# Kernel optimization log

Hardware: AMD Instinct MI355X
Metric: run time of the kernel (lower is better)

Reference implementation:

```python
import jax, jax.numpy as jnp
import numpy as np

SEQ_LEN, N_FEAT, EMB = 512, 8, 64
HID = 2 * EMB  # 128
BATCH = 512


def _lstm_layer(x, Wih, Whh, bih, bhh):
    """Single-layer LSTM, batch_first x: [B,T,F]. PyTorch gate order i,f,g,o.
    Returns (outputs [B,T,H], final hidden [B,H])."""
    B = x.shape[0]
    H = Whh.shape[1]
    # precompute input projections for all timesteps: [B,T,4H]
    xp = jnp.einsum('btf,gf->btg', x, Wih) + bih + bhh

    def step(carry, xt):
        h, c = carry
        gates = xt + h @ Whh.T  # [B,4H]
        i, f, g, o = jnp.split(gates, 4, axis=-1)
        i = jax.nn.sigmoid(i)
        f = jax.nn.sigmoid(f)
        g = jnp.tanh(g)
        o = jax.nn.sigmoid(o)
        c = f * c + i * g
        h = o * jnp.tanh(c)
        return (h, c), h

    h0 = jnp.zeros((B, H), dtype=x.dtype)
    c0 = jnp.zeros((B, H), dtype=x.dtype)
    (hT, _), hs = jax.lax.scan(step, (h0, c0), xp.transpose(1, 0, 2))
    return hs.transpose(1, 0, 2), hT


def setup_inputs() -> dict:
    key = jax.random.key(0)
    ks = jax.random.split(key, 13)
    inp = {"x": jax.random.normal(ks[0], (BATCH, SEQ_LEN, N_FEAT), dtype=jnp.float32)}

    def mk(k, shape, fan):
        s = 1.0 / np.sqrt(fan)
        return jax.random.uniform(k, shape, dtype=jnp.float32, minval=-s, maxval=s)

    # layer 1: in=N_FEAT, hid=HID
    inp["Wih1"] = mk(ks[1], (4 * HID, N_FEAT), HID)
    inp["Whh1"] = mk(ks[2], (4 * HID, HID), HID)
    inp["bih1"] = mk(ks[3], (4 * HID,), HID)
    inp["bhh1"] = mk(ks[4], (4 * HID,), HID)
    # layer 2: in=HID, hid=HID
    inp["Wih2"] = mk(ks[5], (4 * HID, HID), HID)
    inp["Whh2"] = mk(ks[6], (4 * HID, HID), HID)
    inp["bih2"] = mk(ks[7], (4 * HID,), HID)
    inp["bhh2"] = mk(ks[8], (4 * HID,), HID)
    # layer 3: in=HID, hid=EMB
    inp["Wih3"] = mk(ks[9], (4 * EMB, HID), EMB)
    inp["Whh3"] = mk(ks[10], (4 * EMB, EMB), EMB)
    inp["bih3"] = mk(ks[11], (4 * EMB,), EMB)
    inp["bhh3"] = mk(ks[12], (4 * EMB,), EMB)
    return inp


def reference(x, Wih1, Whh1, bih1, bhh1, Wih2, Whh2, bih2, bhh2, Wih3, Whh3, bih3, bhh3):
    B = x.shape[0]
    x = x.reshape(B, SEQ_LEN, N_FEAT)
    x, _ = _lstm_layer(x, Wih1, Whh1, bih1, bhh1)
    x, _ = _lstm_layer(x, Wih2, Whh2, bih2, bhh2)
    _, hT = _lstm_layer(x, Wih3, Whh3, bih3, bhh3)
    return hT  # [B, EMB]
```

## Files before the change

kernel.cpp:

```cpp
#include <hip/hip_runtime.h>


#define DEVI __device__ __forceinline__

typedef _Float16 h8 __attribute__((ext_vector_type(8)));
typedef float f4 __attribute__((ext_vector_type(4)));

static constexpr int T_ = 512, TC_ = 16, NC_ = T_ / TC_;

DEVI float sigmoidf_(float x) {
    return __builtin_amdgcn_rcpf(1.f + __builtin_amdgcn_exp2f(x * -1.44269504f));
}
DEVI float tanhf_(float x) {
    return 2.f * __builtin_amdgcn_rcpf(1.f + __builtin_amdgcn_exp2f(x * -2.88539008f)) - 1.f;
}

DEVI h8 cvt8(const float* p) {
    const float4 a = *reinterpret_cast<const float4*>(p);
    const float4 b = *reinterpret_cast<const float4*>(p + 4);
    return h8{(_Float16)a.x, (_Float16)a.y, (_Float16)a.z, (_Float16)a.w,
              (_Float16)b.x, (_Float16)b.y, (_Float16)b.z, (_Float16)b.w};
}

DEVI void lds_barrier() {
    asm volatile("s_waitcnt lgkmcnt(0)\n\ts_barrier" ::: "memory");
}

template <int LAYER>
DEVI void stage(int tile, char* smem, const float* x, const _Float16* Oin,
                _Float16* Oout, const float* Wih, const float* Whh,
                const float* bih, const float* bhh, float* out,
                int* flag_in, int* flag_out) {
    constexpr int H = (LAYER == 3) ? 64 : 128;
    constexpr int KT_H = H / 32;
    constexpr int KT_X = (LAYER == 1) ? 1 : 4;
    constexpr int HP = H + 8;
    constexpr int NWAVE = (LAYER == 3) ? 4 : 8;

    const int tid  = threadIdx.x;
    const int lane = tid & 63;
    const int wv   = tid >> 6;
    const int lr   = lane & 15;
    const int lk   = lane >> 4;
    const int b0   = tile * 16;
    const bool active = (wv < NWAVE);
    const int jcol = (wv & (NWAVE - 1)) * 16 + lr;

    _Float16 (*h_lds)[16][HP] = (_Float16 (*)[16][HP])smem;

    h8 wbh[4][KT_H], wbx[4][KT_X];
    float bias[4];
    if (active) {
#pragma unroll
        for (int q = 0; q < 4; q++) {
#pragma unroll
            for (int kt = 0; kt < KT_H; kt++)
                wbh[q][kt] = cvt8(Whh + (size_t)(q * H + jcol) * H + kt * 32 + lk * 8);
            if constexpr (LAYER == 1) {
                wbx[q][0] = (lk == 0) ? cvt8(Wih + (size_t)(q * H + jcol) * 8) : h8{};
            } else {
#pragma unroll
                for (int kt = 0; kt < KT_X; kt++)
                    wbx[q][kt] = cvt8(Wih + (size_t)(q * H + jcol) * 128 + kt * 32 + lk * 8);
            }
            bias[q] = bih[q * H + jcol] + bhh[q * H + jcol];
        }
    }

    float c[4] = {0.f, 0.f, 0.f, 0.f};

    for (int i = tid; i < 2 * 16 * HP; i += 512) ((_Float16*)smem)[i] = (_Float16)0;
    __syncthreads();

    auto load_x = [&](int t, h8* xa) {
        if constexpr (LAYER == 1) {
            xa[0] = (lk == 0) ? cvt8(x + ((size_t)(b0 + lr) * T_ + t) * 8) : h8{};
        } else {
#pragma unroll
            for (int kt = 0; kt < KT_X; kt++)
                xa[kt] = *reinterpret_cast<const h8*>(
                    Oin + ((size_t)(b0 + lr) * T_ + t) * 128 + kt * 32 + lk * 8);
        }
    };

    auto xmfma = [&](const h8* xv, f4* ax) {
#pragma unroll
        for (int q = 0; q < 4; q++) ax[q] = f4{bias[q], bias[q], bias[q], bias[q]};
#pragma unroll
        for (int kt = 0; kt < KT_X; kt++)
#pragma unroll
            for (int q = 0; q < 4; q++)
                ax[q] = __builtin_amdgcn_mfma_f32_16x16x32_f16(xv[kt], wbx[q][kt], ax[q], 0, 0, 0);
    };

    h8 xa[KT_X], xb[KT_X];
    f4 accA[4], accB[4];

#define STEP_BODY(T_EXPR, TT, CUR, ACCU, ACCN, XLOAD, XPROJ)                              \
    {                                                                                     \
        const int t = (T_EXPR);                                                           \
        h8 ha[KT_H];                                                                      \
        _Pragma("unroll")                                                                 \
        for (int kt = 0; kt < KT_H; kt++)                                                 \
            ha[kt] = *reinterpret_cast<const h8*>(&h_lds[CUR][lr][kt * 32 + lk * 8]);     \
        _Pragma("unroll")                                                                 \
        for (int kt = 0; kt < KT_H; kt++)                                                 \
            _Pragma("unroll")                                                             \
            for (int q = 0; q < 4; q++)                                                   \
                ACCU[q] = __builtin_amdgcn_mfma_f32_16x16x32_f16(ha[kt], wbh[q][kt],      \
                                                                 ACCU[q], 0, 0, 0);       \
        if ((TT) + 2 < TC_) load_x(t + 2, XLOAD);          \
        _Pragma("unroll")                                                                 \
        for (int i = 0; i < 4; i++) {                                                     \
            const float gi = sigmoidf_(ACCU[0][i]);                                       \
            const float gf = sigmoidf_(ACCU[1][i]);                                       \
            const float gg = tanhf_(ACCU[2][i]);                                          \
            const float go = sigmoidf_(ACCU[3][i]);                                       \
            c[i] = gf * c[i] + gi * gg;                                                   \
            const float h = go * tanhf_(c[i]);                                            \
            const int row = lk * 4 + i;                                                   \
            h_lds[(CUR) ^ 1][row][jcol] = (_Float16)h;                                    \
            if constexpr (LAYER < 3) {                                                    \
                Oout[((size_t)(b0 + row) * T_ + t) * 128 + jcol] = (_Float16)h;           \
            } else {                                                                      \
                if (t == T_ - 1) out[(size_t)(b0 + row) * 64 + jcol] = h;                 \
            }                                                                             \
        }                                                                                 \
        if ((TT) + 1 < TC_) xmfma(XPROJ, ACCN);   \
    }

    for (int ch = 0; ch < NC_; ch++) {
        if constexpr (LAYER > 1) {
            if (tid == 0) {
                while (__hip_atomic_load(flag_in, __ATOMIC_RELAXED,
                                         __HIP_MEMORY_SCOPE_AGENT) < ch + 1)
                    __builtin_amdgcn_s_sleep(2);
                __threadfence();
            }
            __syncthreads();
        }
        const int t0 = ch * TC_;
        if (active) {
            load_x(t0, xa);
            load_x(t0 + 1, xb);
            xmfma(xa, accA);
        }

        for (int tb = 0; tb < TC_ / 2; tb++) {
            if (active) STEP_BODY(t0 + 2 * tb, 2 * tb, 0, accA, accB, xa, xb);
            lds_barrier();
            if (active) STEP_BODY(t0 + 2 * tb + 1, 2 * tb + 1, 1, accB, accA, xb, xa);
            lds_barrier();
        }

        if constexpr (LAYER < 3) {
            asm volatile("s_waitcnt vmcnt(0)" ::: "memory");
            __syncthreads();
            if (tid == 0) {
                __threadfence();
                __hip_atomic_store(flag_out, ch + 1, __ATOMIC_RELAXED,
                                   __HIP_MEMORY_SCOPE_AGENT);
            }
        }
    }
#undef STEP_BODY
}

__global__ __launch_bounds__(512, 1)
void mega_k(const float* __restrict__ x,
            const float* __restrict__ Wih1, const float* __restrict__ Whh1,
            const float* __restrict__ bih1, const float* __restrict__ bhh1,
            const float* __restrict__ Wih2, const float* __restrict__ Whh2,
            const float* __restrict__ bih2, const float* __restrict__ bhh2,
            const float* __restrict__ Wih3, const float* __restrict__ Whh3,
            const float* __restrict__ bih3, const float* __restrict__ bhh3,
            _Float16* __restrict__ O1, _Float16* __restrict__ O2,
            float* __restrict__ out, int* __restrict__ flags) {
    extern __shared__ char smem[];
    const int bid = blockIdx.x;
    if (bid < 32) {
        stage<1>(bid, smem, x, nullptr, O1, Wih1, Whh1, bih1, bhh1, nullptr,
                 nullptr, flags + bid);
    } else if (bid < 64) {
        stage<2>(bid - 32, smem, nullptr, O1, O2, Wih2, Whh2, bih2, bhh2, nullptr,
                 flags + (bid - 32), flags + 32 + (bid - 32));
    } else {
        stage<3>(bid - 64, smem, nullptr, O2, nullptr, Wih3, Whh3, bih3, bhh3, out,
                 flags + 32 + (bid - 64), nullptr);
    }
}

__global__ void zero_flags_k(int* flags) {
    if (threadIdx.x < 64)
        __hip_atomic_store(flags + threadIdx.x, 0, __ATOMIC_RELAXED,
                           __HIP_MEMORY_SCOPE_AGENT);
}

extern "C" void kernel_launch(void* const* d_in, const int* in_sizes, int n_in,
                              void* d_out, int out_size, void* d_ws, size_t ws_size,
                              hipStream_t stream) {
    const float* x = (const float*)d_in[0];
    float* out = (float*)d_out;

    char* ws = (char*)d_ws;
    _Float16* O1 = (_Float16*)ws;
    _Float16* O2 = (_Float16*)(ws + (size_t)67108864);
    int* flags   = (int*)(ws + (size_t)134217728);
    (void)ws_size; (void)in_sizes; (void)n_in; (void)out_size;

    zero_flags_k<<<1, 64, 0, stream>>>(flags);
    mega_k<<<96, 512, 8704, stream>>>(
        x,
        (const float*)d_in[1], (const float*)d_in[2], (const float*)d_in[3], (const float*)d_in[4],
        (const float*)d_in[5], (const float*)d_in[6], (const float*)d_in[7], (const float*)d_in[8],
        (const float*)d_in[9], (const float*)d_in[10], (const float*)d_in[11], (const float*)d_in[12],
        O1, O2, out, flags);
}
```

Before: 723.4 us.

## Process two batch tiles per block to interleave independent LSTM recurrences

```diff
diff --git a/kernel.cpp b/kernel.cpp
--- a/kernel.cpp
+++ b/kernel.cpp
@@ -27,26 +27,28 @@
 }
 
 template <int LAYER>
-DEVI void stage(int tile, char* smem, const float* x, const _Float16* Oin,
-                _Float16* Oout, const float* Wih, const float* Whh,
-                const float* bih, const float* bhh, float* out,
-                int* flag_in, int* flag_out) {
+DEVI void stage2(int tA, int tB, char* smem, const float* x, const _Float16* Oin,
+                 _Float16* Oout, const float* Wih, const float* Whh,
+                 const float* bih, const float* bhh, float* out,
+                 int* flin_base, int* flout_base) {
     constexpr int H = (LAYER == 3) ? 64 : 128;
     constexpr int KT_H = H / 32;
     constexpr int KT_X = (LAYER == 1) ? 1 : 4;
     constexpr int HP = H + 8;
     constexpr int NWAVE = (LAYER == 3) ? 4 : 8;
+    constexpr int LBUF = 2 * 16 * HP;
 
     const int tid  = threadIdx.x;
     const int lane = tid & 63;
     const int wv   = tid >> 6;
     const int lr   = lane & 15;
     const int lk   = lane >> 4;
-    const int b0   = tile * 16;
     const bool active = (wv < NWAVE);
     const int jcol = (wv & (NWAVE - 1)) * 16 + lr;
-
-    _Float16 (*h_lds)[16][HP] = (_Float16 (*)[16][HP])smem;
+    const int bA = tA * 16, bB = tB * 16;
+
+    _Float16 (*hldsA)[16][HP] = (_Float16 (*)[16][HP])smem;
+    _Float16 (*hldsB)[16][HP] = (_Float16 (*)[16][HP])(smem + LBUF * 2);
 
     h8 wbh[4][KT_H], wbx[4][KT_X];
     float bias[4];
@@ -67,12 +69,12 @@
         }
     }
 
-    float c[4] = {0.f, 0.f, 0.f, 0.f};
-
-    for (int i = tid; i < 2 * 16 * HP; i += 512) ((_Float16*)smem)[i] = (_Float16)0;
+    float cA[4] = {0.f, 0.f, 0.f, 0.f}, cB[4] = {0.f, 0.f, 0.f, 0.f};
+
+    for (int i = tid; i < 2 * LBUF; i += 512) ((_Float16*)smem)[i] = (_Float16)0;
     __syncthreads();
 
-    auto load_x = [&](int t, h8* xa) {
+    auto load_x = [&](int b0, int t, h8* xa) {
         if constexpr (LAYER == 1) {
             xa[0] = (lk == 0) ? cvt8(x + ((size_t)(b0 + lr) * T_ + t) * 8) : h8{};
         } else {
@@ -93,46 +95,71 @@
                 ax[q] = __builtin_amdgcn_mfma_f32_16x16x32_f16(xv[kt], wbx[q][kt], ax[q], 0, 0, 0);
     };
 
-    h8 xa[KT_X], xb[KT_X];
+    h8 xsA[KT_X], xsB[KT_X];
     f4 accA[4], accB[4];
 
-#define STEP_BODY(T_EXPR, TT, CUR, ACCU, ACCN, XLOAD, XPROJ)                              \
+#define STEP2(T_EXPR, TT, CUR)                                                            \
     {                                                                                     \
         const int t = (T_EXPR);                                                           \
-        h8 ha[KT_H];                                                                      \
+                   \
+        if ((TT) + 1 < TC_) { load_x(bA, t + 1, xsA); load_x(bB, t + 1, xsB); }           \
+        h8 haA[KT_H], haB[KT_H];                                                          \
         _Pragma("unroll")                                                                 \
-        for (int kt = 0; kt < KT_H; kt++)                                                 \
-            ha[kt] = *reinterpret_cast<const h8*>(&h_lds[CUR][lr][kt * 32 + lk * 8]);     \
+        for (int kt = 0; kt < KT_H; kt++) {                                               \
+            haA[kt] = *reinterpret_cast<const h8*>(&hldsA[CUR][lr][kt * 32 + lk * 8]);    \
+            haB[kt] = *reinterpret_cast<const h8*>(&hldsB[CUR][lr][kt * 32 + lk * 8]);    \
+        }                                                                                 \
         _Pragma("unroll")                                                                 \
         for (int kt = 0; kt < KT_H; kt++)                                                 \
             _Pragma("unroll")                                                             \
-            for (int q = 0; q < 4; q++)                                                   \
-                ACCU[q] = __builtin_amdgcn_mfma_f32_16x16x32_f16(ha[kt], wbh[q][kt],      \
-                                                                 ACCU[q], 0, 0, 0);       \
-        if ((TT) + 2 < TC_) load_x(t + 2, XLOAD);          \
+            for (int q = 0; q < 4; q++) {                                                 \
+                accA[q] = __builtin_amdgcn_mfma_f32_16x16x32_f16(haA[kt], wbh[q][kt],     \
+                                                                 accA[q], 0, 0, 0);       \
+                accB[q] = __builtin_amdgcn_mfma_f32_16x16x32_f16(haB[kt], wbh[q][kt],     \
+                                                                 accB[q], 0, 0, 0);       \
+            }                                                                             \
         _Pragma("unroll")                                                                 \
         for (int i = 0; i < 4; i++) {                                                     \
-            const float gi = sigmoidf_(ACCU[0][i]);                                       \
-            const float gf = sigmoidf_(ACCU[1][i]);                                       \
-            const float gg = tanhf_(ACCU[2][i]);                                          \
-            const float go = sigmoidf_(ACCU[3][i]);                                       \
-            c[i] = gf * c[i] + gi * gg;                                                   \
-            const float h = go * tanhf_(c[i]);                                            \
             const int row = lk * 4 + i;                                                   \
-            h_lds[(CUR) ^ 1][row][jcol] = (_Float16)h;                                    \
-            if constexpr (LAYER < 3) {                                                    \
-                Oout[((size_t)(b0 + row) * T_ + t) * 128 + jcol] = (_Float16)h;           \
-            } else {                                                                      \
-                if (t == T_ - 1) out[(size_t)(b0 + row) * 64 + jcol] = h;                 \
+            {                                                                             \
+                const float gi = sigmoidf_(accA[0][i]);                                   \
+                const float gf = sigmoidf_(accA[1][i]);                                   \
+                const float gg = tanhf_(accA[2][i]);                                      \
+                const float go = sigmoidf_(accA[3][i]);                                   \
+                cA[i] = gf * cA[i] + gi * gg;                                             \
+                const float h = go * tanhf_(cA[i]);                                       \
+                hldsA[(CUR) ^ 1][row][jcol] = (_Float16)h;                                \
+                if constexpr (LAYER < 3) {                                                \
+                    Oout[((size_t)(bA + row) * T_ + t) * 128 + jcol] = (_Float16)h;       \
+                } else {                                                                  \
+                    if (t == T_ - 1) out[(size_t)(bA + row) * 64 + jcol] = h;             \
+                }                                                                         \
+            }                                                                             \
+            {                                                                             \
+                const float gi = sigmoidf_(accB[0][i]);                                   \
+                const float gf = sigmoidf_(accB[1][i]);                                   \
+                const float gg = tanhf_(accB[2][i]);                                      \
+                const float go = sigmoidf_(accB[3][i]);                                   \
+                cB[i] = gf * cB[i] + gi * gg;                                             \
+                const float h = go * tanhf_(cB[i]);                                       \
+                hldsB[(CUR) ^ 1][row][jcol] = (_Float16)h;                                \
+                if constexpr (LAYER < 3) {                                                \
+                    Oout[((size_t)(bB + row) * T_ + t) * 128 + jcol] = (_Float16)h;       \
+                } else {                                                                  \
+                    if (t == T_ - 1) out[(size_t)(bB + row) * 64 + jcol] = h;             \
+                }                                                                         \
             }                                                                             \
         }                                                                                 \
-        if ((TT) + 1 < TC_) xmfma(XPROJ, ACCN);   \
+        if ((TT) + 1 < TC_) { xmfma(xsA, accA); xmfma(xsB, accB); }                       \
     }
 
     for (int ch = 0; ch < NC_; ch++) {
         if constexpr (LAYER > 1) {
             if (tid == 0) {
-                while (__hip_atomic_load(flag_in, __ATOMIC_RELAXED,
+                while (__hip_atomic_load(flin_base + tA, __ATOMIC_RELAXED,
+                                         __HIP_MEMORY_SCOPE_AGENT) < ch + 1)
+                    __builtin_amdgcn_s_sleep(2);
+                while (__hip_atomic_load(flin_base + tB, __ATOMIC_RELAXED,
                                          __HIP_MEMORY_SCOPE_AGENT) < ch + 1)
                     __builtin_amdgcn_s_sleep(2);
                 __threadfence();
@@ -141,15 +168,16 @@
         }
         const int t0 = ch * TC_;
         if (active) {
-            load_x(t0, xa);
-            load_x(t0 + 1, xb);
-            xmfma(xa, accA);
+            load_x(bA, t0, xsA);
+            load_x(bB, t0, xsB);
+            xmfma(xsA, accA);
+            xmfma(xsB, accB);
         }
 
         for (int tb = 0; tb < TC_ / 2; tb++) {
-            if (active) STEP_BODY(t0 + 2 * tb, 2 * tb, 0, accA, accB, xa, xb);
+            if (active) STEP2(t0 + 2 * tb, 2 * tb, 0);
             lds_barrier();
-            if (active) STEP_BODY(t0 + 2 * tb + 1, 2 * tb + 1, 1, accB, accA, xb, xa);
+            if (active) STEP2(t0 + 2 * tb + 1, 2 * tb + 1, 1);
             lds_barrier();
         }
 
@@ -158,15 +186,17 @@
             __syncthreads();
             if (tid == 0) {
                 __threadfence();
-                __hip_atomic_store(flag_out, ch + 1, __ATOMIC_RELAXED,
+                __hip_atomic_store(flout_base + tA, ch + 1, __ATOMIC_RELAXED,
+                                   __HIP_MEMORY_SCOPE_AGENT);
+                __hip_atomic_store(flout_base + tB, ch + 1, __ATOMIC_RELAXED,
                                    __HIP_MEMORY_SCOPE_AGENT);
             }
         }
     }
-#undef STEP_BODY
-}
-
-__global__ __launch_bounds__(512, 1)
+#undef STEP2
+}
+
+__global__ __launch_bounds__(512, 2)
 void mega_k(const float* __restrict__ x,
             const float* __restrict__ Wih1, const float* __restrict__ Whh1,
             const float* __restrict__ bih1, const float* __restrict__ bhh1,
@@ -178,15 +208,17 @@
             float* __restrict__ out, int* __restrict__ flags) {
     extern __shared__ char smem[];
     const int bid = blockIdx.x;
-    if (bid < 32) {
-        stage<1>(bid, smem, x, nullptr, O1, Wih1, Whh1, bih1, bhh1, nullptr,
-                 nullptr, flags + bid);
-    } else if (bid < 64) {
-        stage<2>(bid - 32, smem, nullptr, O1, O2, Wih2, Whh2, bih2, bhh2, nullptr,
-                 flags + (bid - 32), flags + 32 + (bid - 32));
+    if (bid < 16) {
+        stage2<1>(2 * bid, 2 * bid + 1, smem, x, nullptr, O1,
+                  Wih1, Whh1, bih1, bhh1, nullptr, nullptr, flags);
+    } else if (bid < 32) {
+        const int p = bid - 16;
+        stage2<2>(2 * p, 2 * p + 1, smem, nullptr, O1, O2,
+                  Wih2, Whh2, bih2, bhh2, nullptr, flags, flags + 32);
     } else {
-        stage<3>(bid - 64, smem, nullptr, O2, nullptr, Wih3, Whh3, bih3, bhh3, out,
-                 flags + 32 + (bid - 64), nullptr);
+        const int p = bid - 32;
+        stage2<3>(2 * p, 2 * p + 1, smem, nullptr, O2, nullptr,
+                  Wih3, Whh3, bih3, bhh3, out, flags + 32, nullptr);
     }
 }
 
@@ -209,7 +241,7 @@
     (void)ws_size; (void)in_sizes; (void)n_in; (void)out_size;
 
     zero_flags_k<<<1, 64, 0, stream>>>(flags);
-    mega_k<<<96, 512, 8704, stream>>>(
+    mega_k<<<48, 512, 17408, stream>>>(
         x,
         (const float*)d_in[1], (const float*)d_in[2], (const float*)d_in[3], (const float*)d_in[4],
         (const float*)d_in[5], (const float*)d_in[6], (const float*)d_in[7], (const float*)d_in[8],
```

Result: slower. 1.745 ms (+141.2%).

## Split input projection and recurrence into paired waves using LDS handoff

Applied to the files above, without the earlier changes.

```diff
diff --git a/kernel.cpp b/kernel.cpp
--- a/kernel.cpp
+++ b/kernel.cpp
@@ -8,12 +8,8 @@
 
 static constexpr int T_ = 512, TC_ = 16, NC_ = T_ / TC_;
 
-DEVI float sigmoidf_(float x) {
-    return __builtin_amdgcn_rcpf(1.f + __builtin_amdgcn_exp2f(x * -1.44269504f));
-}
-DEVI float tanhf_(float x) {
-    return 2.f * __builtin_amdgcn_rcpf(1.f + __builtin_amdgcn_exp2f(x * -2.88539008f)) - 1.f;
-}
+DEVI float rcpf_(float x) { return __builtin_amdgcn_rcpf(x); }
+DEVI float exp2f_(float x) { return __builtin_amdgcn_exp2f(x); }
 
 DEVI h8 cvt8(const float* p) {
     const float4 a = *reinterpret_cast<const float4*>(p);
@@ -35,98 +31,122 @@
     constexpr int KT_H = H / 32;
     constexpr int KT_X = (LAYER == 1) ? 1 : 4;
     constexpr int HP = H + 8;
-    constexpr int NWAVE = (LAYER == 3) ? 4 : 8;
-
-    const int tid  = threadIdx.x;
-    const int lane = tid & 63;
-    const int wv   = tid >> 6;
-    const int lr   = lane & 15;
-    const int lk   = lane >> 4;
-    const int b0   = tile * 16;
-    const bool active = (wv < NWAVE);
-    const int jcol = (wv & (NWAVE - 1)) * 16 + lr;
+    constexpr int NJG = H / 16;
+
+    const int tid = threadIdx.x, lane = tid & 63, wv = tid >> 6;
+    const int lr = lane & 15, lk = lane >> 4;
+    const int b0 = tile * 16;
+    const int isx = wv & 1;
+    const int jg = wv >> 1;
+    const bool act = (jg < NJG);
+    const int jcol = jg * 16 + lr;
 
     _Float16 (*h_lds)[16][HP] = (_Float16 (*)[16][HP])smem;
-
-    h8 wbh[4][KT_H], wbx[4][KT_X];
-    float bias[4];
-    if (active) {
-#pragma unroll
-        for (int q = 0; q < 4; q++) {
+    float* pacc = (float*)(smem + 8704);
+
+    h8 wreg[16];
+    f4 acc[4];
+    h8 tmp8[4];
+    float state[4] = {0.f, 0.f, 0.f, 0.f};
+
+    if (act) {
+        if (!isx) {
 #pragma unroll
             for (int kt = 0; kt < KT_H; kt++)
-                wbh[q][kt] = cvt8(Whh + (size_t)(q * H + jcol) * H + kt * 32 + lk * 8);
-            if constexpr (LAYER == 1) {
-                wbx[q][0] = (lk == 0) ? cvt8(Wih + (size_t)(q * H + jcol) * 8) : h8{};
-            } else {
-#pragma unroll
-                for (int kt = 0; kt < KT_X; kt++)
-                    wbx[q][kt] = cvt8(Wih + (size_t)(q * H + jcol) * 128 + kt * 32 + lk * 8);
+#pragma unroll
+                for (int q = 0; q < 4; q++)
+                    wreg[kt * 4 + q] = cvt8(Whh + (size_t)(q * H + jcol) * H + kt * 32 + lk * 8);
+        } else {
+#pragma unroll
+            for (int q = 0; q < 4; q++) {
+                if constexpr (LAYER == 1) {
+                    wreg[q] = (lk == 0) ? cvt8(Wih + (size_t)(q * H + jcol) * 8) : h8{};
+                } else {
+#pragma unroll
+                    for (int kt = 0; kt < KT_X; kt++)
+                        wreg[q * KT_X + kt] = cvt8(Wih + (size_t)(q * H + jcol) * 128 + kt * 32 + lk * 8);
+                }
+                state[q] = bih[q * H + jcol] + bhh[q * H + jcol];
             }
-            bias[q] = bih[q * H + jcol] + bhh[q * H + jcol];
-        }
-    }
-
-    float c[4] = {0.f, 0.f, 0.f, 0.f};
-
-    for (int i = tid; i < 2 * 16 * HP; i += 512) ((_Float16*)smem)[i] = (_Float16)0;
+        }
+    }
+
+    for (int i = tid; i < 2 * 16 * HP; i += 1024) ((_Float16*)smem)[i] = (_Float16)0;
     __syncthreads();
 
-    auto load_x = [&](int t, h8* xa) {
+    auto load_x = [&](int t) {
         if constexpr (LAYER == 1) {
-            xa[0] = (lk == 0) ? cvt8(x + ((size_t)(b0 + lr) * T_ + t) * 8) : h8{};
+            tmp8[0] = (lk == 0) ? cvt8(x + ((size_t)(b0 + lr) * T_ + t) * 8) : h8{};
         } else {
 #pragma unroll
             for (int kt = 0; kt < KT_X; kt++)
-                xa[kt] = *reinterpret_cast<const h8*>(
+                tmp8[kt] = *reinterpret_cast<const h8*>(
                     Oin + ((size_t)(b0 + lr) * T_ + t) * 128 + kt * 32 + lk * 8);
         }
     };
-
-    auto xmfma = [&](const h8* xv, f4* ax) {
-#pragma unroll
-        for (int q = 0; q < 4; q++) ax[q] = f4{bias[q], bias[q], bias[q], bias[q]};
+    auto xproj = [&](int par) {
+#pragma unroll
+        for (int q = 0; q < 4; q++) acc[q] = f4{state[q], state[q], state[q], state[q]};
 #pragma unroll
         for (int kt = 0; kt < KT_X; kt++)
 #pragma unroll
             for (int q = 0; q < 4; q++)
-                ax[q] = __builtin_amdgcn_mfma_f32_16x16x32_f16(xv[kt], wbx[q][kt], ax[q], 0, 0, 0);
+                acc[q] = __builtin_amdgcn_mfma_f32_16x16x32_f16(tmp8[kt], wreg[q * KT_X + kt],
+                                                                acc[q], 0, 0, 0);
+#pragma unroll
+        for (int q = 0; q < 4; q++)
+            *reinterpret_cast<f4*>(pacc + ((size_t)((par * 8 + jg) * 4 + q)) * 256 + lane * 4) = acc[q];
     };
 
-    h8 xa[KT_X], xb[KT_X];
-    f4 accA[4], accB[4];
-
-#define STEP_BODY(T_EXPR, TT, CUR, ACCU, ACCN, XLOAD, XPROJ)                              \
+#define STEP(TT_EXPR, PAR)                                                                \
     {                                                                                     \
-        const int t = (T_EXPR);                                                           \
-        h8 ha[KT_H];                                                                      \
-        _Pragma("unroll")                                                                 \
-        for (int kt = 0; kt < KT_H; kt++)                                                 \
-            ha[kt] = *reinterpret_cast<const h8*>(&h_lds[CUR][lr][kt * 32 + lk * 8]);     \
-        _Pragma("unroll")                                                                 \
-        for (int kt = 0; kt < KT_H; kt++)                                                 \
-            _Pragma("unroll")                                                             \
-            for (int q = 0; q < 4; q++)                                                   \
-                ACCU[q] = __builtin_amdgcn_mfma_f32_16x16x32_f16(ha[kt], wbh[q][kt],      \
-                                                                 ACCU[q], 0, 0, 0);       \
-        if ((TT) + 2 < TC_) load_x(t + 2, XLOAD);          \
-        _Pragma("unroll")                                                                 \
-        for (int i = 0; i < 4; i++) {                                                     \
-            const float gi = sigmoidf_(ACCU[0][i]);                                       \
-            const float gf = sigmoidf_(ACCU[1][i]);                                       \
-            const float gg = tanhf_(ACCU[2][i]);                                          \
-            const float go = sigmoidf_(ACCU[3][i]);                                       \
-            c[i] = gf * c[i] + gi * gg;                                                   \
-            const float h = go * tanhf_(c[i]);                                            \
-            const int row = lk * 4 + i;                                                   \
-            h_lds[(CUR) ^ 1][row][jcol] = (_Float16)h;                                    \
-            if constexpr (LAYER < 3) {                                                    \
-                Oout[((size_t)(b0 + row) * T_ + t) * 128 + jcol] = (_Float16)h;           \
+        const int tt = (TT_EXPR);                                                         \
+        const int t = t0 + tt;                                                            \
+        if (act) {                                                                        \
+            if (!isx) {                                                                   \
+                _Pragma("unroll")                                                         \
+                for (int q = 0; q < 4; q++)                                               \
+                    acc[q] = *reinterpret_cast<const f4*>(                                \
+                        pacc + ((size_t)(((PAR) * 8 + jg) * 4 + q)) * 256 + lane * 4);    \
+                _Pragma("unroll")                                                         \
+                for (int kt = 0; kt < KT_H; kt++)                                         \
+                    tmp8[kt] = *reinterpret_cast<const h8*>(&h_lds[PAR][lr][kt * 32 + lk * 8]); \
+                _Pragma("unroll")                                                         \
+                for (int kt = 0; kt < KT_H; kt++)                                         \
+                    _Pragma("unroll")                                                     \
+                    for (int q = 0; q < 4; q++)                                           \
+                        acc[q] = __builtin_amdgcn_mfma_f32_16x16x32_f16(tmp8[kt],         \
+                                     wreg[kt * 4 + q], acc[q], 0, 0, 0);                  \
+                float e0[4], e1[4], e2[4], e3[4];                                         \
+                _Pragma("unroll")                                                         \
+                for (int i = 0; i < 4; i++) {                                             \
+                    e0[i] = exp2f_(acc[0][i] * -1.44269504f);                             \
+                    e1[i] = exp2f_(acc[1][i] * -1.44269504f);                             \
+                    e2[i] = exp2f_(acc[2][i] * -2.88539008f);                             \
+                    e3[i] = exp2f_(acc[3][i] * -1.44269504f);                             \
+                }                                                                         \
+                _Pragma("unroll")                                                         \
+                for (int i = 0; i < 4; i++) {                                             \
+                    const float gi = rcpf_(1.f + e0[i]);                                  \
+                    const float gf = rcpf_(1.f + e1[i]);                                  \
+                    const float gg = 2.f * rcpf_(1.f + e2[i]) - 1.f;                      \
+                    const float go = rcpf_(1.f + e3[i]);                                  \
+                    state[i] = gf * state[i] + gi * gg;                                   \
+                    const float th = 2.f * rcpf_(1.f + exp2f_(state[i] * -2.88539008f)) - 1.f; \
+                    const float h = go * th;                                              \
+                    const int row = lk * 4 + i;                                           \
+                    h_lds[(PAR) ^ 1][row][jcol] = (_Float16)h;                            \
+                    if constexpr (LAYER < 3) {                                            \
+                        Oout[((size_t)(b0 + row) * T_ + t) * 128 + jcol] = (_Float16)h;   \
+                    } else {                                                              \
+                        if (t == T_ - 1) out[(size_t)(b0 + row) * 64 + jcol] = h;         \
+                    }                                                                     \
+                }                                                                         \
             } else {                                                                      \
-                if (t == T_ - 1) out[(size_t)(b0 + row) * 64 + jcol] = h;                 \
+                if (tt < TC_ - 1) xproj((PAR) ^ 1);               \
+                if (tt < TC_ - 2) load_x(t + 2);                  \
             }                                                                             \
         }                                                                                 \
-        if ((TT) + 1 < TC_) xmfma(XPROJ, ACCN);   \
     }
 
     for (int ch = 0; ch < NC_; ch++) {
@@ -137,19 +157,21 @@
                     __builtin_amdgcn_s_sleep(2);
                 __threadfence();
             }
-            __syncthreads();
-        }
+        }
+        __syncthreads();
         const int t0 = ch * TC_;
-        if (active) {
-            load_x(t0, xa);
-            load_x(t0 + 1, xb);
-            xmfma(xa, accA);
-        }
+
+        if (act && isx) {
+            load_x(t0);
+            xproj(0);
+            load_x(t0 + 1);
+        }
+        lds_barrier();
 
         for (int tb = 0; tb < TC_ / 2; tb++) {
-            if (active) STEP_BODY(t0 + 2 * tb, 2 * tb, 0, accA, accB, xa, xb);
+            STEP(2 * tb, 0)
             lds_barrier();
-            if (active) STEP_BODY(t0 + 2 * tb + 1, 2 * tb + 1, 1, accB, accA, xb, xa);
+            STEP(2 * tb + 1, 1)
             lds_barrier();
         }
 
@@ -163,10 +185,10 @@
             }
         }
     }
-#undef STEP_BODY
-}
-
-__global__ __launch_bounds__(512, 1)
+#undef STEP
+}
+
+__global__ __launch_bounds__(1024)
 void mega_k(const float* __restrict__ x,
             const float* __restrict__ Wih1, const float* __restrict__ Whh1,
             const float* __restrict__ bih1, const float* __restrict__ bhh1,
@@ -209,7 +231,7 @@
     (void)ws_size; (void)in_sizes; (void)n_in; (void)out_size;
 
     zero_flags_k<<<1, 64, 0, stream>>>(flags);
-    mega_k<<<96, 512, 8704, stream>>>(
+    mega_k<<<96, 1024, 74240, stream>>>(
         x,
         (const float*)d_in[1], (const float*)d_in[2], (const float*)d_in[3], (const float*)d_in[4],
         (const float*)d_in[5], (const float*)d_in[6], (const float*)d_in[7], (const float*)d_in[8],
```

Measured after the change: 906.7 us. 25.3% more time.
